# Optimization experiments

Measured on AMD Instinct MI355X. Metric: run time of the kernel, lower is better.

Reference implementation:

```python
import jax, jax.numpy as jnp
import numpy as np

BATCH, SEQ, D_IN, D_OUT, N_EXP, RANK, TOP_K = 8, 2048, 1024, 1024, 8, 32, 2


def setup_inputs() -> dict:
    key = jax.random.key(0)
    ks = jax.random.split(key, 9)
    x = jax.random.normal(ks[0], (BATCH, SEQ, D_IN), jnp.float32)
    base_W = jax.random.normal(ks[1], (D_OUT, D_IN), jnp.float32) * (1.0 / np.sqrt(D_IN))
    base_b = jax.random.normal(ks[2], (D_OUT,), jnp.float32) * 0.02
    router_W = jax.random.normal(ks[3], (N_EXP, D_IN), jnp.float32) * 0.02
    router_b = jax.random.normal(ks[4], (N_EXP,), jnp.float32) * 0.02
    A = jax.random.normal(ks[5], (N_EXP, RANK, D_IN), jnp.float32) * 0.02
    S_a = jax.random.normal(ks[6], (N_EXP, RANK, D_IN), jnp.float32)
    B = jax.random.normal(ks[7], (N_EXP, D_OUT, RANK), jnp.float32) * 0.02
    S_b = jax.random.normal(ks[8], (N_EXP, D_OUT, RANK), jnp.float32)
    return {"x": x, "base_W": base_W, "base_b": base_b,
            "router_W": router_W, "router_b": router_b,
            "A": A, "S_a": S_a, "B": B, "S_b": S_b}


def reference(x, base_W, base_b, router_W, router_b, A, S_a, B, S_b):
    # Flatten tokens: [T, d_in]
    x2 = x.reshape(-1, x.shape[-1])
    T = x2.shape[0]
    E = router_W.shape[0]

    # Base linear: y0 = x W^T + b
    base_out = x2 @ base_W.T + base_b

    # Router: softmax over experts, then top-k
    logits = x2 @ router_W.T + router_b          # [T, E]
    probs = jax.nn.softmax(logits, axis=-1)
    top_vals, top_idx = jax.lax.top_k(probs, TOP_K)  # [T, k]

    # Dense gate matrix: gate[t, e] = routed prob if e in top-k of token t else 0
    gate = jnp.zeros((T, E), x2.dtype).at[jnp.arange(T)[:, None], top_idx].add(top_vals)

    # Sigmoid-masked low-rank factors
    A_t = A * jax.nn.sigmoid(S_a)                # [E, r, d_in]
    B_t = B * jax.nn.sigmoid(S_b)                # [E, d_out, r]

    # Expert residuals, gated and summed (gate folded at rank dim to stay small)
    h = jnp.einsum('td,erd->ter', x2, A_t)       # [T, E, r]
    hg = h * gate[:, :, None]                    # [T, E, r]
    delta = jnp.einsum('ter,eor->to', hg, B_t)   # [T, d_out]

    y = (base_out + delta).reshape(*x.shape[:-1], base_W.shape[0])
    return y
```

## Files before the change

### kernel.cpp

```cpp
#include <hip/hip_runtime.h>
#include <hip/hip_bf16.h>
#include <math.h>

#define TT   16384
#define DIN  1024
#define DOUT 1024
#define NEXP 8
#define RANK 32
#define KCAT 256

using bf16 = __hip_bfloat16;
typedef __attribute__((ext_vector_type(8))) short short8;
typedef __attribute__((ext_vector_type(4))) short short4v;
typedef __attribute__((ext_vector_type(4))) float f32x4;

static __device__ __forceinline__ float b2f(bf16 v) { return __bfloat162float(v); }
static __device__ __forceinline__ bf16  f2b(float v) { return __float2bfloat16(v); }

static __device__ __forceinline__ void load_lds16(const bf16* g, bf16* l) {
  __builtin_amdgcn_global_load_lds(
      (const __attribute__((address_space(1))) void*)g,
      (__attribute__((address_space(3))) void*)l, 16, 0, 0);
}

__global__ __launch_bounds__(256) void cvt_kernel(const float* __restrict__ in,
                                                  bf16* __restrict__ out, int n4) {
  for (int i = blockIdx.x * blockDim.x + threadIdx.x; i < n4;
       i += gridDim.x * blockDim.x) {
    float4 v = ((const float4*)in)[i];
    union { short4v s; bf16 b[4]; } u;
    u.b[0] = f2b(v.x); u.b[1] = f2b(v.y); u.b[2] = f2b(v.z); u.b[3] = f2b(v.w);
    ((short4v*)out)[i] = u.s;
  }
}

__global__ __launch_bounds__(256) void prep_kernel(const float* __restrict__ A,
                                                   const float* __restrict__ Sa,
                                                   const float* __restrict__ B,
                                                   const float* __restrict__ Sb,
                                                   bf16* __restrict__ Acat,
                                                   bf16* __restrict__ BcatT) {
  const int n = NEXP * RANK * DIN;
  for (int idx = blockIdx.x * blockDim.x + threadIdx.x; idx < n;
       idx += gridDim.x * blockDim.x) {
    float a = A[idx];
    float s = Sa[idx];
    Acat[idx] = f2b(a * (1.0f / (1.0f + __expf(-s))));
    int o = idx >> 8;
    int j = idx & 255;
    int e = j >> 5, r = j & 31;
    int src = e * (DOUT * RANK) + o * RANK + r;
    float bb = B[src];
    float sb = Sb[src];
    BcatT[idx] = f2b(bb * (1.0f / (1.0f + __expf(-sb))));
  }
}

__global__ __launch_bounds__(64) void router_kernel(const bf16* __restrict__ xb,
                                                    const float* __restrict__ rW,
                                                    const float* __restrict__ rb,
                                                    float* __restrict__ gate) {
  const int t = blockIdx.x;
  const int lane = threadIdx.x;
  const bf16* xrow = xb + (size_t)t * DIN;
  const int base = lane * 16;
  float xv[16];
  {
    short8 x0 = *(const short8*)&xrow[base];
    short8 x1 = *(const short8*)&xrow[base + 8];
    #pragma unroll
    for (int j = 0; j < 8; ++j) {
      union { short s; bf16 b; } u0, u1;
      u0.s = x0[j]; u1.s = x1[j];
      xv[j] = b2f(u0.b); xv[8 + j] = b2f(u1.b);
    }
  }
  float acc[NEXP] = {};
  #pragma unroll
  for (int e = 0; e < NEXP; ++e) {
    const float4* w4 = (const float4*)&rW[e * DIN + base];
    #pragma unroll
    for (int q = 0; q < 4; ++q) {
      float4 w = w4[q];
      acc[e] += xv[q * 4 + 0] * w.x + xv[q * 4 + 1] * w.y +
                xv[q * 4 + 2] * w.z + xv[q * 4 + 3] * w.w;
    }
  }
  #pragma unroll
  for (int e = 0; e < NEXP; ++e) {
    #pragma unroll
    for (int off = 32; off > 0; off >>= 1)
      acc[e] += __shfl_down(acc[e], off);
  }
  if (lane == 0) {
    float lg[NEXP];
    float mx = -1e30f;
    #pragma unroll
    for (int e = 0; e < NEXP; ++e) { lg[e] = acc[e] + rb[e]; mx = fmaxf(mx, lg[e]); }
    float se = 0.f;
    #pragma unroll
    for (int e = 0; e < NEXP; ++e) { lg[e] = __expf(lg[e] - mx); se += lg[e]; }
    float inv = 1.0f / se;
    int i1 = 0;
    #pragma unroll
    for (int e = 1; e < NEXP; ++e) if (lg[e] > lg[i1]) i1 = e;
    int i2 = (i1 == 0) ? 1 : 0;
    #pragma unroll
    for (int e = 0; e < NEXP; ++e) if (e != i1 && lg[e] > lg[i2]) i2 = e;
    #pragma unroll
    for (int e = 0; e < NEXP; ++e)
      gate[(size_t)t * NEXP + e] = (e == i1 || e == i2) ? lg[e] * inv : 0.0f;
  }
}

__global__ __launch_bounds__(256) void gemm1_kernel(const bf16* __restrict__ xb,
                                                    const bf16* __restrict__ Acat,
                                                    const float* __restrict__ gate,
                                                    bf16* __restrict__ hg) {
  __shared__ alignas(16) bf16 As[128][32];
  __shared__ alignas(16) bf16 Bs[64][32];
  const int tid = threadIdx.x, wid = tid >> 6, lane = tid & 63;
  const int wr = wid >> 1, wc = wid & 1;
  const int tileRow = blockIdx.x * 128, tileCol = blockIdx.y * 64;
  f32x4 acc[4][2] = {};

  for (int kt = 0; kt < DIN / 32; ++kt) {
    const int k0 = kt * 32;
    const int srow = (lane >> 2);
    const int scol = (lane & 3) * 8;
    #pragma unroll
    for (int i = 0; i < 2; ++i) {
      int row = i * 64 + wid * 16 + srow;
      load_lds16(xb + (size_t)(tileRow + row) * DIN + k0 + scol, &As[i * 64 + wid * 16][0]);
    }
    {
      int row = wid * 16 + srow;
      load_lds16(Acat + (size_t)(tileCol + row) * DIN + k0 + scol, &Bs[wid * 16][0]);
    }
    __syncthreads();
    short8 a[4], b[2];
    #pragma unroll
    for (int m = 0; m < 4; ++m)
      a[m] = *(const short8*)&As[wr * 64 + m * 16 + (lane & 15)][(lane >> 4) * 8];
    #pragma unroll
    for (int n = 0; n < 2; ++n)
      b[n] = *(const short8*)&Bs[wc * 32 + n * 16 + (lane & 15)][(lane >> 4) * 8];
    #pragma unroll
    for (int m = 0; m < 4; ++m)
      #pragma unroll
      for (int n = 0; n < 2; ++n)
        acc[m][n] = __builtin_amdgcn_mfma_f32_16x16x32_bf16(a[m], b[n], acc[m][n], 0, 0, 0);
    __syncthreads();
  }

  #pragma unroll
  for (int n = 0; n < 2; ++n) {
    int j = tileCol + wc * 32 + n * 16 + (lane & 15);
    int e = j >> 5;
    #pragma unroll
    for (int m = 0; m < 4; ++m) {
      int row0 = tileRow + wr * 64 + m * 16 + (lane >> 4) * 4;
      #pragma unroll
      for (int r = 0; r < 4; ++r) {
        float g = gate[(size_t)(row0 + r) * NEXP + e];
        hg[(size_t)(row0 + r) * KCAT + j] = f2b(acc[m][n][r] * g);
      }
    }
  }
}

__global__ __launch_bounds__(256) void gemm2_kernel(const bf16* __restrict__ xb,
                                                    const bf16* __restrict__ Wb,
                                                    const float* __restrict__ bias,
                                                    const bf16* __restrict__ hg,
                                                    const bf16* __restrict__ BcatT,
                                                    float* __restrict__ out) {
  __shared__ alignas(16) bf16 As[128][32];
  __shared__ alignas(16) bf16 Bs[128][32];
  const int tid = threadIdx.x, wid = tid >> 6, lane = tid & 63;
  const int wr = wid >> 1, wc = wid & 1;
  const int tileRow = blockIdx.x * 128, tileCol = blockIdx.y * 128;
  f32x4 acc[4][4] = {};

  const int KT = (DIN + KCAT) / 32;
  for (int kt = 0; kt < KT; ++kt) {
    const bf16 *aptr, *bptr;
    int lda, k0;
    if (kt < DIN / 32) { aptr = xb; bptr = Wb;    lda = DIN;  k0 = kt * 32; }
    else               { aptr = hg; bptr = BcatT; lda = KCAT; k0 = (kt - DIN / 32) * 32; }
    const int srow = (lane >> 2);
    const int scol = (lane & 3) * 8;
    #pragma unroll
    for (int i = 0; i < 2; ++i) {
      int row = i * 64 + wid * 16 + srow;
      load_lds16(aptr + (size_t)(tileRow + row) * lda + k0 + scol, &As[i * 64 + wid * 16][0]);
    }
    #pragma unroll
    for (int i = 0; i < 2; ++i) {
      int row = i * 64 + wid * 16 + srow;
      load_lds16(bptr + (size_t)(tileCol + row) * lda + k0 + scol, &Bs[i * 64 + wid * 16][0]);
    }
    __syncthreads();
    short8 a[4], b[4];
    #pragma unroll
    for (int m = 0; m < 4; ++m)
      a[m] = *(const short8*)&As[wr * 64 + m * 16 + (lane & 15)][(lane >> 4) * 8];
    #pragma unroll
    for (int n = 0; n < 4; ++n)
      b[n] = *(const short8*)&Bs[wc * 64 + n * 16 + (lane & 15)][(lane >> 4) * 8];
    #pragma unroll
    for (int m = 0; m < 4; ++m)
      #pragma unroll
      for (int n = 0; n < 4; ++n)
        acc[m][n] = __builtin_amdgcn_mfma_f32_16x16x32_bf16(a[m], b[n], acc[m][n], 0, 0, 0);
    __syncthreads();
  }

  #pragma unroll
  for (int n = 0; n < 4; ++n) {
    int col = tileCol + wc * 64 + n * 16 + (lane & 15);
    float bb = bias[col];
    #pragma unroll
    for (int m = 0; m < 4; ++m) {
      int row0 = tileRow + wr * 64 + m * 16 + (lane >> 4) * 4;
      #pragma unroll
      for (int r = 0; r < 4; ++r)
        out[(size_t)(row0 + r) * DOUT + col] = acc[m][n][r] + bb;
    }
  }
}

extern "C" void kernel_launch(void* const* d_in, const int* in_sizes, int n_in,
                              void* d_out, int out_size, void* d_ws, size_t ws_size,
                              hipStream_t stream) {
  const float* x  = (const float*)d_in[0];
  const float* W  = (const float*)d_in[1];
  const float* bb = (const float*)d_in[2];
  const float* rW = (const float*)d_in[3];
  const float* rb = (const float*)d_in[4];
  const float* A  = (const float*)d_in[5];
  const float* Sa = (const float*)d_in[6];
  const float* B  = (const float*)d_in[7];
  const float* Sb = (const float*)d_in[8];
  float* out = (float*)d_out;

  char* ws = (char*)d_ws;
  float* gate  = (float*)ws;
  bf16*  Acat  = (bf16*)(ws + (512 << 10));
  bf16*  BcatT = (bf16*)(ws + (1024 << 10));
  bf16*  Wb    = (bf16*)(ws + (1536 << 10));
  bf16*  hg    = (bf16*)(ws + (3584 << 10));
  bf16*  xb    = (bf16*)(ws + (11776 << 10));

  cvt_kernel<<<2048, 256, 0, stream>>>(x, xb, TT * DIN / 4);
  cvt_kernel<<<512, 256, 0, stream>>>(W, Wb, DOUT * DIN / 4);
  prep_kernel<<<512, 256, 0, stream>>>(A, Sa, B, Sb, Acat, BcatT);
  router_kernel<<<TT, 64, 0, stream>>>(xb, rW, rb, gate);
  gemm1_kernel<<<dim3(TT / 128, KCAT / 64), 256, 0, stream>>>(xb, Acat, gate, hg);
  gemm2_kernel<<<dim3(TT / 128, DOUT / 128), 256, 0, stream>>>(xb, Wb, bb, hg, BcatT, out);
}
```

Before: 248.8 us.

## Fuse x conversion into router, double K tile with XOR-swizzled LDS staging

The x fp32-to-bf16 conversion is folded into the router kernel, so x is read once for both conversion and routing logits and one launch plus a bf16 re-read disappear. Both GEMMs now stage 64-wide K tiles instead of 32, which halves the number of barrier pairs per K loop. They also store 16-byte chunks in LDS with an XOR swizzle to avoid bank conflicts on the MFMA operand reads. The cost is more LDS per block, which may reduce occupancy, and more complex swizzle addressing.

```diff
diff --git a/kernel.cpp b/kernel.cpp
--- a/kernel.cpp
+++ b/kernel.cpp
@@ -21,6 +21,13 @@
   __builtin_amdgcn_global_load_lds(
       (const __attribute__((address_space(1))) void*)g,
       (__attribute__((address_space(3))) void*)l, 16, 0, 0);
+}
+
+static __device__ __forceinline__ void stage_swz(const bf16* gRowBase, size_t lda,
+                                                 bf16* ldsRowBase, int lane) {
+  const int r = lane >> 3;
+  const int c = (lane & 7) ^ r;
+  load_lds16(gRowBase + (size_t)r * lda + c * 8, ldsRowBase);
 }
 
 __global__ __launch_bounds__(256) void cvt_kernel(const float* __restrict__ in,
@@ -56,32 +63,32 @@
   }
 }
 
-__global__ __launch_bounds__(64) void router_kernel(const bf16* __restrict__ xb,
-                                                    const float* __restrict__ rW,
-                                                    const float* __restrict__ rb,
-                                                    float* __restrict__ gate) {
-  const int t = blockIdx.x;
-  const int lane = threadIdx.x;
-  const bf16* xrow = xb + (size_t)t * DIN;
-  const int base = lane * 16;
+__global__ __launch_bounds__(256) void cvtrouter_kernel(const float* __restrict__ x,
+                                                        const float* __restrict__ rW,
+                                                        const float* __restrict__ rb,
+                                                        bf16* __restrict__ xb,
+                                                        float* __restrict__ gate) {
+  const int wid = threadIdx.x >> 6, lane = threadIdx.x & 63;
+  const int t = blockIdx.x * 4 + wid;
+  const float* xrow = x + (size_t)t * DIN;
+  bf16* xbrow = xb + (size_t)t * DIN;
+
   float xv[16];
-  {
-    short8 x0 = *(const short8*)&xrow[base];
-    short8 x1 = *(const short8*)&xrow[base + 8];
-    #pragma unroll
-    for (int j = 0; j < 8; ++j) {
-      union { short s; bf16 b; } u0, u1;
-      u0.s = x0[j]; u1.s = x1[j];
-      xv[j] = b2f(u0.b); xv[8 + j] = b2f(u1.b);
-    }
-  }
+  #pragma unroll
+  for (int q = 0; q < 4; ++q) {
+    float4 v = *(const float4*)&xrow[q * 256 + lane * 4];
+    xv[q * 4 + 0] = v.x; xv[q * 4 + 1] = v.y; xv[q * 4 + 2] = v.z; xv[q * 4 + 3] = v.w;
+    union { short4v s; bf16 b[4]; } u;
+    u.b[0] = f2b(v.x); u.b[1] = f2b(v.y); u.b[2] = f2b(v.z); u.b[3] = f2b(v.w);
+    *(short4v*)&xbrow[q * 256 + lane * 4] = u.s;
+  }
+
   float acc[NEXP] = {};
   #pragma unroll
   for (int e = 0; e < NEXP; ++e) {
-    const float4* w4 = (const float4*)&rW[e * DIN + base];
     #pragma unroll
     for (int q = 0; q < 4; ++q) {
-      float4 w = w4[q];
+      float4 w = *(const float4*)&rW[e * DIN + q * 256 + lane * 4];
       acc[e] += xv[q * 4 + 0] * w.x + xv[q * 4 + 1] * w.y +
                 xv[q * 4 + 2] * w.z + xv[q * 4 + 3] * w.w;
     }
@@ -90,7 +97,7 @@
   for (int e = 0; e < NEXP; ++e) {
     #pragma unroll
     for (int off = 32; off > 0; off >>= 1)
-      acc[e] += __shfl_down(acc[e], off);
+      acc[e] += __shfl_xor(acc[e], off);
   }
   if (lane == 0) {
     float lg[NEXP];
@@ -117,39 +124,42 @@
                                                     const bf16* __restrict__ Acat,
                                                     const float* __restrict__ gate,
                                                     bf16* __restrict__ hg) {
-  __shared__ alignas(16) bf16 As[128][32];
-  __shared__ alignas(16) bf16 Bs[64][32];
+  __shared__ alignas(16) bf16 As[128][64];
+  __shared__ alignas(16) bf16 Bs[64][64];
   const int tid = threadIdx.x, wid = tid >> 6, lane = tid & 63;
   const int wr = wid >> 1, wc = wid & 1;
   const int tileRow = blockIdx.x * 128, tileCol = blockIdx.y * 64;
   f32x4 acc[4][2] = {};
 
-  for (int kt = 0; kt < DIN / 32; ++kt) {
-    const int k0 = kt * 32;
-    const int srow = (lane >> 2);
-    const int scol = (lane & 3) * 8;
+  for (int kt = 0; kt < DIN / 64; ++kt) {
+    const int k0 = kt * 64;
+    #pragma unroll
+    for (int i = 0; i < 4; ++i) {
+      int br = wid * 32 + i * 8;
+      stage_swz(xb + (size_t)(tileRow + br) * DIN + k0, DIN, &As[br][0], lane);
+    }
     #pragma unroll
     for (int i = 0; i < 2; ++i) {
-      int row = i * 64 + wid * 16 + srow;
-      load_lds16(xb + (size_t)(tileRow + row) * DIN + k0 + scol, &As[i * 64 + wid * 16][0]);
-    }
-    {
-      int row = wid * 16 + srow;
-      load_lds16(Acat + (size_t)(tileCol + row) * DIN + k0 + scol, &Bs[wid * 16][0]);
-    }
-    __syncthreads();
-    short8 a[4], b[2];
-    #pragma unroll
-    for (int m = 0; m < 4; ++m)
-      a[m] = *(const short8*)&As[wr * 64 + m * 16 + (lane & 15)][(lane >> 4) * 8];
-    #pragma unroll
-    for (int n = 0; n < 2; ++n)
-      b[n] = *(const short8*)&Bs[wc * 32 + n * 16 + (lane & 15)][(lane >> 4) * 8];
-    #pragma unroll
-    for (int m = 0; m < 4; ++m)
+      int br = wid * 16 + i * 8;
+      stage_swz(Acat + (size_t)(tileCol + br) * DIN + k0, DIN, &Bs[br][0], lane);
+    }
+    __syncthreads();
+    #pragma unroll
+    for (int ks = 0; ks < 2; ++ks) {
+      const int pcA = ((ks * 4) + (lane >> 4)) ^ (lane & 7);
+      short8 a[4], b[2];
+      #pragma unroll
+      for (int m = 0; m < 4; ++m)
+        a[m] = *(const short8*)&As[wr * 64 + m * 16 + (lane & 15)][pcA * 8];
       #pragma unroll
       for (int n = 0; n < 2; ++n)
-        acc[m][n] = __builtin_amdgcn_mfma_f32_16x16x32_bf16(a[m], b[n], acc[m][n], 0, 0, 0);
+        b[n] = *(const short8*)&Bs[wc * 32 + n * 16 + (lane & 15)][pcA * 8];
+      #pragma unroll
+      for (int m = 0; m < 4; ++m)
+        #pragma unroll
+        for (int n = 0; n < 2; ++n)
+          acc[m][n] = __builtin_amdgcn_mfma_f32_16x16x32_bf16(a[m], b[n], acc[m][n], 0, 0, 0);
+    }
     __syncthreads();
   }
 
@@ -175,46 +185,44 @@
                                                     const bf16* __restrict__ hg,
                                                     const bf16* __restrict__ BcatT,
                                                     float* __restrict__ out) {
-  __shared__ alignas(16) bf16 As[128][32];
-  __shared__ alignas(16) bf16 Bs[128][32];
+  __shared__ alignas(16) bf16 As[128][64];
+  __shared__ alignas(16) bf16 Bs[128][64];
   const int tid = threadIdx.x, wid = tid >> 6, lane = tid & 63;
   const int wr = wid >> 1, wc = wid & 1;
   const int tileRow = blockIdx.x * 128, tileCol = blockIdx.y * 128;
   f32x4 acc[4][4] = {};
 
-  const int KT = (DIN + KCAT) / 32;
-  for (int kt = 0; kt < KT; ++kt) {
-    const bf16 *aptr, *bptr;
-    int lda, k0;
-    if (kt < DIN / 32) { aptr = xb; bptr = Wb;    lda = DIN;  k0 = kt * 32; }
-    else               { aptr = hg; bptr = BcatT; lda = KCAT; k0 = (kt - DIN / 32) * 32; }
-    const int srow = (lane >> 2);
-    const int scol = (lane & 3) * 8;
-    #pragma unroll
-    for (int i = 0; i < 2; ++i) {
-      int row = i * 64 + wid * 16 + srow;
-      load_lds16(aptr + (size_t)(tileRow + row) * lda + k0 + scol, &As[i * 64 + wid * 16][0]);
-    }
-    #pragma unroll
-    for (int i = 0; i < 2; ++i) {
-      int row = i * 64 + wid * 16 + srow;
-      load_lds16(bptr + (size_t)(tileCol + row) * lda + k0 + scol, &Bs[i * 64 + wid * 16][0]);
-    }
-    __syncthreads();
-    short8 a[4], b[4];
-    #pragma unroll
-    for (int m = 0; m < 4; ++m)
-      a[m] = *(const short8*)&As[wr * 64 + m * 16 + (lane & 15)][(lane >> 4) * 8];
-    #pragma unroll
-    for (int n = 0; n < 4; ++n)
-      b[n] = *(const short8*)&Bs[wc * 64 + n * 16 + (lane & 15)][(lane >> 4) * 8];
-    #pragma unroll
-    for (int m = 0; m < 4; ++m)
+  auto tile_step = [&](const bf16* aptr, const bf16* bptr, size_t lda, int k0) {
+    #pragma unroll
+    for (int i = 0; i < 4; ++i) {
+      int br = wid * 32 + i * 8;
+      stage_swz(aptr + (size_t)(tileRow + br) * lda + k0, lda, &As[br][0], lane);
+      stage_swz(bptr + (size_t)(tileCol + br) * lda + k0, lda, &Bs[br][0], lane);
+    }
+    __syncthreads();
+    #pragma unroll
+    for (int ks = 0; ks < 2; ++ks) {
+      const int pc = ((ks * 4) + (lane >> 4)) ^ (lane & 7);
+      short8 a[4], b[4];
+      #pragma unroll
+      for (int m = 0; m < 4; ++m)
+        a[m] = *(const short8*)&As[wr * 64 + m * 16 + (lane & 15)][pc * 8];
       #pragma unroll
       for (int n = 0; n < 4; ++n)
-        acc[m][n] = __builtin_amdgcn_mfma_f32_16x16x32_bf16(a[m], b[n], acc[m][n], 0, 0, 0);
-    __syncthreads();
-  }
+        b[n] = *(const short8*)&Bs[wc * 64 + n * 16 + (lane & 15)][pc * 8];
+      #pragma unroll
+      for (int m = 0; m < 4; ++m)
+        #pragma unroll
+        for (int n = 0; n < 4; ++n)
+          acc[m][n] = __builtin_amdgcn_mfma_f32_16x16x32_bf16(a[m], b[n], acc[m][n], 0, 0, 0);
+    }
+    __syncthreads();
+  };
+
+  for (int kt = 0; kt < DIN / 64; ++kt)
+    tile_step(xb, Wb, DIN, kt * 64);
+  for (int kt = 0; kt < KCAT / 64; ++kt)
+    tile_step(hg, BcatT, KCAT, kt * 64);
 
   #pragma unroll
   for (int n = 0; n < 4; ++n) {
@@ -252,10 +260,9 @@
   bf16*  hg    = (bf16*)(ws + (3584 << 10));
   bf16*  xb    = (bf16*)(ws + (11776 << 10));
 
-  cvt_kernel<<<2048, 256, 0, stream>>>(x, xb, TT * DIN / 4);
   cvt_kernel<<<512, 256, 0, stream>>>(W, Wb, DOUT * DIN / 4);
   prep_kernel<<<512, 256, 0, stream>>>(A, Sa, B, Sb, Acat, BcatT);
-  router_kernel<<<TT, 64, 0, stream>>>(xb, rW, rb, gate);
+  cvtrouter_kernel<<<TT / 4, 256, 0, stream>>>(x, rW, rb, xb, gate);
   gemm1_kernel<<<dim3(TT / 128, KCAT / 64), 256, 0, stream>>>(xb, Acat, gate, hg);
   gemm2_kernel<<<dim3(TT / 128, DOUT / 128), 256, 0, stream>>>(xb, Wb, bb, hg, BcatT, out);
 }
```

Result: faster. 217.4 us (-12.6%).
